# Kernel optimization log

Measured on AMD Instinct MI355X. Metric: run time of the kernel, lower is better.

Reference implementation:

```python
import jax, jax.numpy as jnp
import numpy as np

B, S, D_IN, D_OUT = 4, 4096, 256, 256

def setup_inputs() -> dict:
    key = jax.random.key(0)
    ks = jax.random.split(key, 7)
    scale = 1.0 / np.sqrt(D_IN)
    return {
        "x": jax.random.normal(ks[0], (B, S, D_IN), dtype=jnp.float32),
        "Wq": jax.random.uniform(ks[1], (D_IN, D_OUT), jnp.float32, -scale, scale),
        "bq": jax.random.uniform(ks[2], (D_OUT,), jnp.float32, -scale, scale),
        "Wk": jax.random.uniform(ks[3], (D_IN, D_OUT), jnp.float32, -scale, scale),
        "bk": jax.random.uniform(ks[4], (D_OUT,), jnp.float32, -scale, scale),
        "Wv": jax.random.uniform(ks[5], (D_IN, D_OUT), jnp.float32, -scale, scale),
        "bv": jax.random.uniform(ks[6], (D_OUT,), jnp.float32, -scale, scale),
    }

def reference(x, Wq, bq, Wk, bk, Wv, bv):
    # QKV projections: [B, S, D_OUT]
    q = jnp.einsum("bsd,de->bse", x, Wq) + bq
    k = jnp.einsum("bsd,de->bse", x, Wk) + bk
    v = jnp.einsum("bsd,de->bse", x, Wv) + bv
    # Scaled dot-product attention; full [B, S, S] scores as in the original.
    scores = jnp.einsum("bqe,bke->bqk", q, k) / jnp.sqrt(jnp.asarray(q.shape[-1], q.dtype))
    attn = jax.nn.softmax(scores, axis=-1)
    return jnp.einsum("bqk,bke->bqe", attn, v)
```

## Files before the change

### kernel.cpp

```cpp
#include <hip/hip_runtime.h>
#include <stdint.h>

typedef unsigned short u16;
typedef __attribute__((ext_vector_type(4))) float f32x4;
typedef __attribute__((ext_vector_type(8))) short bf16x8;
typedef __attribute__((ext_vector_type(4))) int i32x4;
typedef __attribute__((ext_vector_type(2))) unsigned int u32x2;

#define SEQ 4096
#define DIM 256
#define QSCALE 0.09016844f

__device__ __forceinline__ u16 f2bf(float f) {
  union { float f; uint32_t u; } v; v.f = f;
  uint32_t r = (v.u + 0x7FFFu + ((v.u >> 16) & 1u)) >> 16;
  return (u16)r;
}

__device__ __forceinline__ void gload_lds16(const void* g, void* lds) {
  __builtin_amdgcn_global_load_lds(
      (const __attribute__((address_space(1))) uint32_t*)g,
      (__attribute__((address_space(3))) uint32_t*)lds, 16, 0, 0);
}

__global__ __launch_bounds__(256) void wt_kernel(const float* __restrict__ Wq,
                                                 const float* __restrict__ Wk,
                                                 const float* __restrict__ Wv,
                                                 u16* __restrict__ wt) {
  int b = blockIdx.x;
  int w = b >> 8;
  int n = b & 255;
  const float* W = (w == 0) ? Wq : ((w == 1) ? Wk : Wv);
  float scale = (w == 0) ? QSCALE : 1.0f;
  int k = threadIdx.x;
  wt[(w * 256 + n) * 256 + k] = f2bf(W[k * 256 + n] * scale);
}

__global__ __launch_bounds__(256) void qkv_kernel(
    const float* __restrict__ x, const float* __restrict__ bq,
    const float* __restrict__ bk, const float* __restrict__ bv,
    const u16* __restrict__ wt, u16* __restrict__ qs, u16* __restrict__ kk,
    char* __restrict__ vt) {
  __shared__ __align__(16) u16 lds_b[16384];
  __shared__ __align__(16) u16 lds_v[4096];
  int tid = threadIdx.x;
  int w = tid >> 6, l = tid & 63;
  int a = l & 15, g = l >> 4;
  int rowbase = blockIdx.x * 64;

  bf16x8 afr[8];
  {
    int row = rowbase + w * 16 + a;
    const float* xr = x + (size_t)row * 256;
#pragma unroll
    for (int ks = 0; ks < 8; ++ks) {
      int k0 = ks * 32 + g * 8;
      union { bf16x8 s; u16 u[8]; } fr;
#pragma unroll
      for (int i = 0; i < 8; ++i) fr.u[i] = f2bf(xr[k0 + i]);
      afr[ks] = fr.s;
    }
  }

  for (int w3 = 0; w3 < 3; ++w3) {
    const float* bias = (w3 == 0) ? bq : ((w3 == 1) ? bk : bv);
    for (int qn = 0; qn < 4; ++qn) {
      {
        const u16* src = wt + (w3 * 256 + qn * 64) * 256;
        for (int j = 0; j < 8; ++j) {
          uint32_t inst = w * 8 + j;
          uint32_t flat = inst * 1024 + l * 16;
          uint32_t row = flat >> 9;
          uint32_t c5 = (flat >> 4) & 31;
          uint32_t sc = (c5 & ~7u) | ((c5 ^ row) & 7u);
          gload_lds16(src + row * 256 + sc * 8, ((char*)lds_b) + inst * 1024);
        }
      }
      __syncthreads();
      f32x4 acc[4];
#pragma unroll
      for (int n0 = 0; n0 < 4; ++n0) acc[n0] = (f32x4){0.f, 0.f, 0.f, 0.f};
#pragma unroll
      for (int ks = 0; ks < 8; ++ks) {
#pragma unroll
        for (int n0 = 0; n0 < 4; ++n0) {
          uint32_t row = n0 * 16 + a;
          uint32_t c5 = ks * 4 + g;
          uint32_t sc = (c5 & ~7u) | ((c5 ^ row) & 7u);
          bf16x8 bfr = *(const bf16x8*)((const char*)lds_b + row * 512 + sc * 16);
          acc[n0] = __builtin_amdgcn_mfma_f32_16x16x32_bf16(afr[ks], bfr, acc[n0], 0, 0, 0);
        }
      }
      if (w3 < 2) {
        u16* out = (w3 == 0) ? qs : kk;
        float bscale = (w3 == 0) ? QSCALE : 1.0f;
#pragma unroll
        for (int n0 = 0; n0 < 4; ++n0) {
          int col = qn * 64 + n0 * 16 + a;
          float bb = bias[col] * bscale;
#pragma unroll
          for (int r = 0; r < 4; ++r) {
            int row = rowbase + w * 16 + g * 4 + r;
            out[(size_t)row * 256 + col] = f2bf(acc[n0][r] + bb);
          }
        }
      } else {
#pragma unroll
        for (int n0 = 0; n0 < 4; ++n0) {
          int col = qn * 64 + n0 * 16 + a;
          float bb = bias[col];
          int dl = n0 * 16 + a;
#pragma unroll
          for (int r = 0; r < 4; ++r) {
            int m = w * 16 + g * 4 + r;
            uint32_t byteoff =
                (uint32_t)dl * 128 + ((((uint32_t)m >> 3) ^ ((uint32_t)dl & 7)) << 4) + (m & 7) * 2;
            *(u16*)((char*)lds_v + byteoff) = f2bf(acc[n0][r] + bb);
          }
        }
        __syncthreads();
        {
          int dl = tid >> 2;
          size_t base = (size_t)blockIdx.x * 32768 + (size_t)(qn * 64 + dl) * 128;
#pragma unroll
          for (int cc = 0; cc < 2; ++cc) {
            uint32_t c = (tid & 3) + cc * 4;
            i32x4 vd = *(const i32x4*)((const char*)lds_v + dl * 128 + ((c ^ (dl & 7)) << 4));
            *(i32x4*)(vt + base + c * 16) = vd;
          }
        }
      }
      __syncthreads();
    }
  }
}

__device__ __forceinline__ void stage4(const char* src, char* ldsbase,
                                       const uint32_t* so, int w) {
#pragma unroll
  for (int j = 0; j < 4; ++j)
    gload_lds16(src + so[j], ldsbase + (w * 4 + j) * 1024);
}

#define TILE(CUR)                                                              \
  {                                                                            \
    asm volatile("s_waitcnt vmcnt(0) lgkmcnt(0)" ::: "memory");                \
    __builtin_amdgcn_s_barrier();                                              \
    __builtin_amdgcn_sched_barrier(0);                                         \
    if (tcur + 1 < nt) {                                                       \
      stage4(kstp, lds + ((CUR) ^ 1) * 32768, kso, w);                         \
      stage4(vstp, lds + 65536 + ((CUR) ^ 1) * 32768, vso, w);                 \
    }                                                                          \
    kstp += 32768;                                                             \
    vstp += 32768;                                                             \
    f32x4 sc[2][2];                                                            \
    _Pragma("unroll") for (int mt = 0; mt < 2; ++mt)                           \
    _Pragma("unroll") for (int n = 0; n < 2; ++n)                              \
        sc[mt][n] = (f32x4){0.f, 0.f, 0.f, 0.f};                               \
    __builtin_amdgcn_s_setprio(1);                                             \
    _Pragma("unroll") for (int n = 0; n < 2; ++n)                              \
    _Pragma("unroll") for (int j = 0; j < 8; ++j) {                            \
      bf16x8 kfr = *(const bf16x8*)(lds + (CUR) * 32768 + kro[j] + n * 8192);  \
      sc[0][n] = __builtin_amdgcn_mfma_f32_16x16x32_bf16(kfr, qfr[0][j], sc[0][n], 0, 0, 0); \
      sc[1][n] = __builtin_amdgcn_mfma_f32_16x16x32_bf16(kfr, qfr[1][j], sc[1][n], 0, 0, 0); \
    }                                                                          \
    __builtin_amdgcn_s_setprio(0);                                             \
    _Pragma("unroll") for (int mt = 0; mt < 2; ++mt)                           \
    _Pragma("unroll") for (int n = 0; n < 2; ++n) {                            \
      float e0 = exp2f(fminf(sc[mt][n][0], 43.f));                             \
      float e1 = exp2f(fminf(sc[mt][n][1], 43.f));                             \
      float e2 = exp2f(fminf(sc[mt][n][2], 43.f));                             \
      float e3 = exp2f(fminf(sc[mt][n][3], 43.f));                             \
      uint32_t p0 = (uint32_t)f2bf(e0) | ((uint32_t)f2bf(e1) << 16);           \
      uint32_t p1 = (uint32_t)f2bf(e2) | ((uint32_t)f2bf(e3) << 16);           \
      u32x2 pk = {p0, p1};                                                     \
      *(u32x2*)(lds + pwo[n] + mt * 2048) = pk;                                \
    }                                                                          \
    asm volatile("s_waitcnt lgkmcnt(0)" ::: "memory");                         \
    __builtin_amdgcn_s_barrier();                                              \
    __builtin_amdgcn_sched_barrier(0);                                         \
    bf16x8 pfr[2][2];                                                          \
    _Pragma("unroll") for (int mt = 0; mt < 2; ++mt)                           \
    _Pragma("unroll") for (int j2 = 0; j2 < 2; ++j2)                           \
        pfr[mt][j2] = *(const bf16x8*)(lds + pro[j2] + mt * 2048);             \
    __builtin_amdgcn_s_setprio(1);                                             \
    _Pragma("unroll") for (int mt = 0; mt < 2; ++mt)                           \
    _Pragma("unroll") for (int j2 = 0; j2 < 2; ++j2)                           \
        lacc[mt] = __builtin_amdgcn_mfma_f32_16x16x32_bf16(pfr[mt][j2], ones,  \
                                                           lacc[mt], 0, 0, 0); \
    _Pragma("unroll") for (int d0 = 0; d0 < 8; ++d0)                           \
    _Pragma("unroll") for (int j2 = 0; j2 < 2; ++j2) {                         \
      bf16x8 vfr = *(const bf16x8*)(lds + 65536 + (CUR) * 32768 + vro[j2] +    \
                                    d0 * 2048);                                \
      o[0][d0] = __builtin_amdgcn_mfma_f32_16x16x32_bf16(pfr[0][j2], vfr, o[0][d0], 0, 0, 0); \
      o[1][d0] = __builtin_amdgcn_mfma_f32_16x16x32_bf16(pfr[1][j2], vfr, o[1][d0], 0, 0, 0); \
    }                                                                          \
    __builtin_amdgcn_s_setprio(0);                                             \
    ++tcur;                                                                    \
  }

__global__ __launch_bounds__(512, 1) void attn_kernel(
    const u16* __restrict__ qs, const u16* __restrict__ kk,
    const char* __restrict__ vt, float* __restrict__ out,
    float* __restrict__ pOB, float* __restrict__ pl, int split) {
  __shared__ __align__(16) char lds[147456];
  int tid = threadIdx.x;
  int w = tid >> 6, l = tid & 63;
  int a = l & 15, g = l >> 4;
  int qq = w >> 1, sub = w & 1;
  int bx = blockIdx.x;
  int h, batch, qt;
  if (split == 2) { h = bx & 1; batch = (bx >> 1) & 3; qt = bx >> 3; }
  else            { h = 0;      batch = (bx >> 1) & 3; qt = ((bx >> 3) << 1) | (bx & 1); }
  int nt = (split == 2) ? 32 : 64;

  uint32_t a7 = a & 7;
  uint32_t kro[8], vro[2], pro[2], pwo[2], kso[4], vso[4];
#pragma unroll
  for (int j = 0; j < 8; ++j) {
    uint32_t c5 = j * 4 + g;
    kro[j] = (uint32_t)(sub * 32 + a) * 512 +
             (((c5 & ~7u) | ((c5 ^ a7) & 7u)) << 4);
  }
#pragma unroll
  for (int j2 = 0; j2 < 2; ++j2)
    vro[j2] = (uint32_t)(sub * 128 + a) * 128 +
              ((((uint32_t)(j2 * 4 + g)) ^ a7) << 4);
#pragma unroll
  for (int j2 = 0; j2 < 2; ++j2)
    pro[j2] = 131072u + (uint32_t)(qq * 32 + a) * 128 +
              ((((uint32_t)(j2 * 4 + g)) ^ a7) << 4);
#pragma unroll
  for (int n = 0; n < 2; ++n)
    pwo[n] = 131072u + (uint32_t)(qq * 32 + a) * 128 +
             ((((uint32_t)(sub * 4 + n * 2 + (g >> 1))) ^ a7) << 4) + (g & 1) * 8;
#pragma unroll
  for (int j = 0; j < 4; ++j) {
    uint32_t inst = w * 4 + j, flat = inst * 1024 + l * 16;
    {
      uint32_t row = flat >> 9, c5 = (flat >> 4) & 31;
      kso[j] = row * 512 + (((c5 & ~7u) | ((c5 ^ row) & 7u)) << 4);
    }
    {
      uint32_t row = flat >> 7, c3 = (flat >> 4) & 7;
      vso[j] = row * 128 + ((c3 ^ (row & 7)) << 4);
    }
  }

  bf16x8 qfr[2][8];
  {
    const char* qp = (const char*)qs + (size_t)(batch * SEQ + qt * 128) * 512;
#pragma unroll
    for (int mt = 0; mt < 2; ++mt)
#pragma unroll
      for (int j = 0; j < 8; ++j)
        qfr[mt][j] = *(const bf16x8*)(qp + (size_t)(qq * 32 + mt * 16 + a) * 512 +
                                      j * 64 + g * 16);
  }

  f32x4 o[2][8];
  f32x4 lacc[2];
#pragma unroll
  for (int mt = 0; mt < 2; ++mt) {
    lacc[mt] = (f32x4){0.f, 0.f, 0.f, 0.f};
#pragma unroll
    for (int d0 = 0; d0 < 8; ++d0) o[mt][d0] = (f32x4){0.f, 0.f, 0.f, 0.f};
  }
  const short ob = (short)0x3F80;
  bf16x8 ones = {ob, ob, ob, ob, ob, ob, ob, ob};

  const char* kstp = (const char*)kk + (size_t)batch * SEQ * 512 + (size_t)h * 2048 * 512;
  const char* vstp = vt + (size_t)batch * 64 * 32768 + (size_t)h * 32 * 32768;

  stage4(kstp, lds, kso, w);
  stage4(vstp, lds + 65536, vso, w);
  kstp += 32768;
  vstp += 32768;

  int tcur = 0;
  int ntHalf = nt >> 1;
  for (int tp = 0; tp < ntHalf; ++tp) {
    TILE(0)
    TILE(1)
  }

  float* po = (h == 0) ? out : pOB;
  size_t obase = (size_t)(batch * SEQ + qt * 128 + qq * 32) * 256 + sub * 128;
#pragma unroll
  for (int mt = 0; mt < 2; ++mt)
#pragma unroll
    for (int r = 0; r < 4; ++r) {
#pragma unroll
      for (int d0 = 0; d0 < 8; ++d0)
        po[obase + (size_t)(mt * 16 + g * 4 + r) * 256 + d0 * 16 + a] = o[mt][d0][r];
    }
  if (a == 0 && sub == 0) {
#pragma unroll
    for (int mt = 0; mt < 2; ++mt)
#pragma unroll
      for (int r = 0; r < 4; ++r)
        pl[h * 16384 + (batch * 32 + qt) * 128 + qq * 32 + mt * 16 + g * 4 + r] =
            lacc[mt][r];
  }
}

__global__ __launch_bounds__(256) void combine_kernel(float* __restrict__ out,
                                                      const float* __restrict__ pOB,
                                                      const float* __restrict__ pl,
                                                      int split) {
  int b = blockIdx.x;
  int tid = threadIdx.x;
  int batch = b >> 12;
  int rem = b & 4095;
  int qt = rem >> 7, ql = rem & 127;
  size_t idx = (size_t)b * 256 + tid;
  int li = (batch * 32 + qt) * 128 + ql;
  float lA = pl[li];
  float v;
  if (split == 2) {
    float lB = pl[16384 + li];
    v = (out[idx] + pOB[idx]) / (lA + lB);
  } else {
    v = out[idx] / lA;
  }
  out[idx] = v;
}

extern "C" void kernel_launch(void* const* d_in, const int* in_sizes, int n_in,
                              void* d_out, int out_size, void* d_ws, size_t ws_size,
                              hipStream_t stream) {
  const float* x = (const float*)d_in[0];
  const float* Wq = (const float*)d_in[1];
  const float* bq = (const float*)d_in[2];
  const float* Wk = (const float*)d_in[3];
  const float* bk = (const float*)d_in[4];
  const float* Wv = (const float*)d_in[5];
  const float* bv = (const float*)d_in[6];
  char* ws = (char*)d_ws;
  u16* wt = (u16*)ws;
  u16* qs = (u16*)(ws + 0x60000);
  u16* kk = (u16*)(ws + 0x860000);
  char* vt = ws + 0x1060000;
  float* pl = (float*)(ws + 0x1860000);
  float* pOB = (float*)(ws + 0x1880000);
  int split = (ws_size >= 0x2880000ull) ? 2 : 1;
  wt_kernel<<<dim3(768), dim3(256), 0, stream>>>(Wq, Wk, Wv, wt);
  qkv_kernel<<<dim3(256), dim3(256), 0, stream>>>(x, bq, bk, bv, wt, qs, kk, vt);
  attn_kernel<<<dim3(split * 128), dim3(512), 0, stream>>>(qs, kk, vt, (float*)d_out,
                                                           pOB, pl, split);
  combine_kernel<<<dim3(16384), dim3(256), 0, stream>>>((float*)d_out, pOB, pl, split);
}
```

Baseline: 131.4 us.

## Software-pipeline QK and PV stages across tiles to drop mid-tile barrier

Restructures the attention inner loop so that the PV product of tile t-1 runs in the same step as the QK^T and exp of tile t. The P buffer and the V stage are double-buffered, and V for a tile is now loaded one step later than K. This removes the second barrier inside each tile and lets the MFMA work of the two stages interleave. In exchange, LDS grows to 160KB, and a prologue and epilogue are added to handle the first QK step and the last PV step.

```diff
diff --git a/kernel.cpp b/kernel.cpp
--- a/kernel.cpp
+++ b/kernel.cpp
@@ -142,15 +142,34 @@
     gload_lds16(src + so[j], ldsbase + (w * 4 + j) * 1024);
 }
 
-#define TILE(CUR)                                                              \
+#define PV_STEP(SLOT)                                                          \
+  {                                                                            \
+    bf16x8 pfr[2][2];                                                          \
+    _Pragma("unroll") for (int mt = 0; mt < 2; ++mt)                           \
+    _Pragma("unroll") for (int j2 = 0; j2 < 2; ++j2)                           \
+        pfr[mt][j2] = *(const bf16x8*)(lds + (SLOT) * 16384 + pro[j2] + mt * 2048); \
+    __builtin_amdgcn_s_setprio(1);                                             \
+    _Pragma("unroll") for (int mt = 0; mt < 2; ++mt)                           \
+    _Pragma("unroll") for (int j2 = 0; j2 < 2; ++j2)                           \
+        lacc[mt] = __builtin_amdgcn_mfma_f32_16x16x32_bf16(pfr[mt][j2], ones,  \
+                                                           lacc[mt], 0, 0, 0); \
+    _Pragma("unroll") for (int d0 = 0; d0 < 8; ++d0)                           \
+    _Pragma("unroll") for (int j2 = 0; j2 < 2; ++j2) {                         \
+      bf16x8 vfr = *(const bf16x8*)(lds + 65536 + (SLOT) * 32768 + vro[j2] +   \
+                                    d0 * 2048);                                \
+      o[0][d0] = __builtin_amdgcn_mfma_f32_16x16x32_bf16(pfr[0][j2], vfr, o[0][d0], 0, 0, 0); \
+      o[1][d0] = __builtin_amdgcn_mfma_f32_16x16x32_bf16(pfr[1][j2], vfr, o[1][d0], 0, 0, 0); \
+    }                                                                          \
+    __builtin_amdgcn_s_setprio(0);                                             \
+  }
+
+#define TILE(CUR, DO_PV, DO_K)                                                 \
   {                                                                            \
     asm volatile("s_waitcnt vmcnt(0) lgkmcnt(0)" ::: "memory");                \
     __builtin_amdgcn_s_barrier();                                              \
     __builtin_amdgcn_sched_barrier(0);                                         \
-    if (tcur + 1 < nt) {                                                       \
-      stage4(kstp, lds + ((CUR) ^ 1) * 32768, kso, w);                         \
-      stage4(vstp, lds + 65536 + ((CUR) ^ 1) * 32768, vso, w);                 \
-    }                                                                          \
+    stage4(vstp, lds + 65536 + (CUR) * 32768, vso, w);   \
+    if (DO_K) stage4(kstp, lds + ((CUR) ^ 1) * 32768, kso, w);  \
     kstp += 32768;                                                             \
     vstp += 32768;                                                             \
     f32x4 sc[2][2];                                                            \
@@ -174,36 +193,16 @@
       uint32_t p0 = (uint32_t)f2bf(e0) | ((uint32_t)f2bf(e1) << 16);           \
       uint32_t p1 = (uint32_t)f2bf(e2) | ((uint32_t)f2bf(e3) << 16);           \
       u32x2 pk = {p0, p1};                                                     \
-      *(u32x2*)(lds + pwo[n] + mt * 2048) = pk;                                \
+      *(u32x2*)(lds + (CUR) * 16384 + pwo[n] + mt * 2048) = pk;                \
     }                                                                          \
-    asm volatile("s_waitcnt lgkmcnt(0)" ::: "memory");                         \
-    __builtin_amdgcn_s_barrier();                                              \
-    __builtin_amdgcn_sched_barrier(0);                                         \
-    bf16x8 pfr[2][2];                                                          \
-    _Pragma("unroll") for (int mt = 0; mt < 2; ++mt)                           \
-    _Pragma("unroll") for (int j2 = 0; j2 < 2; ++j2)                           \
-        pfr[mt][j2] = *(const bf16x8*)(lds + pro[j2] + mt * 2048);             \
-    __builtin_amdgcn_s_setprio(1);                                             \
-    _Pragma("unroll") for (int mt = 0; mt < 2; ++mt)                           \
-    _Pragma("unroll") for (int j2 = 0; j2 < 2; ++j2)                           \
-        lacc[mt] = __builtin_amdgcn_mfma_f32_16x16x32_bf16(pfr[mt][j2], ones,  \
-                                                           lacc[mt], 0, 0, 0); \
-    _Pragma("unroll") for (int d0 = 0; d0 < 8; ++d0)                           \
-    _Pragma("unroll") for (int j2 = 0; j2 < 2; ++j2) {                         \
-      bf16x8 vfr = *(const bf16x8*)(lds + 65536 + (CUR) * 32768 + vro[j2] +    \
-                                    d0 * 2048);                                \
-      o[0][d0] = __builtin_amdgcn_mfma_f32_16x16x32_bf16(pfr[0][j2], vfr, o[0][d0], 0, 0, 0); \
-      o[1][d0] = __builtin_amdgcn_mfma_f32_16x16x32_bf16(pfr[1][j2], vfr, o[1][d0], 0, 0, 0); \
-    }                                                                          \
-    __builtin_amdgcn_s_setprio(0);                                             \
-    ++tcur;                                                                    \
+    if (DO_PV) PV_STEP((CUR) ^ 1)                                              \
   }
 
 __global__ __launch_bounds__(512, 1) void attn_kernel(
     const u16* __restrict__ qs, const u16* __restrict__ kk,
     const char* __restrict__ vt, float* __restrict__ out,
     float* __restrict__ pOB, float* __restrict__ pl, int split) {
-  __shared__ __align__(16) char lds[147456];
+  __shared__ __align__(16) char lds[163840];
   int tid = threadIdx.x;
   int w = tid >> 6, l = tid & 63;
   int a = l & 15, g = l >> 4;
@@ -212,7 +211,7 @@
   int h, batch, qt;
   if (split == 2) { h = bx & 1; batch = (bx >> 1) & 3; qt = bx >> 3; }
   else            { h = 0;      batch = (bx >> 1) & 3; qt = ((bx >> 3) << 1) | (bx & 1); }
-  int nt = (split == 2) ? 32 : 64;
+  int ntHalf = (split == 2) ? 16 : 32;
 
   uint32_t a7 = a & 7;
   uint32_t kro[8], vro[2], pro[2], pwo[2], kso[4], vso[4];
@@ -273,16 +272,19 @@
   const char* vstp = vt + (size_t)batch * 64 * 32768 + (size_t)h * 32 * 32768;
 
   stage4(kstp, lds, kso, w);
-  stage4(vstp, lds + 65536, vso, w);
   kstp += 32768;
-  vstp += 32768;
-
-  int tcur = 0;
-  int ntHalf = nt >> 1;
-  for (int tp = 0; tp < ntHalf; ++tp) {
-    TILE(0)
-    TILE(1)
-  }
+
+  TILE(0, false, true)
+  for (int tp = 0; tp < ntHalf - 1; ++tp) {
+    TILE(1, true, true)
+    TILE(0, true, true)
+  }
+  TILE(1, true, false)
+
+  asm volatile("s_waitcnt vmcnt(0) lgkmcnt(0)" ::: "memory");
+  __builtin_amdgcn_s_barrier();
+  __builtin_amdgcn_sched_barrier(0);
+  PV_STEP(1)
 
   float* po = (h == 0) ? out : pOB;
   size_t obase = (size_t)(batch * SEQ + qt * 128 + qq * 32) * 256 + sub * 128;
```

New measurement: 129.1 us. No clear change (-1.8%).
